# Kernel tuning notes

Measured on AMD Instinct MI355X. Metric: run time of the kernel, lower is better.

Reference implementation:

```python
import jax, jax.numpy as jnp
import numpy as np

# ---- config (matches init_kwargs) ----
VOCAB = 50000
D_MODEL = 256
N_HEADS = 8
N_LAYERS = 2
N_KERNELS = 11
D_FF = 2048  # torch TransformerEncoderLayer default
D_HEAD = D_MODEL // N_HEADS
LN_EPS = 1e-5


def kernel_mus(n):
    mus = [1.0]
    bin_size = 2.0 / (n - 1)
    mus.append(1 - bin_size / 2)
    for i in range(1, n - 1):
        mus.append(mus[i] - bin_size)
    return mus


def kernel_sigmas(n):
    bin_size = 2.0 / (n - 1)
    return [0.0001] + [0.5 * bin_size] * (n - 1)

MU = jnp.asarray(kernel_mus(N_KERNELS), dtype=jnp.float32)      # [K]
SIGMA = jnp.asarray(kernel_sigmas(N_KERNELS), dtype=jnp.float32)  # [K]


def pos_encoding(seq_len, d):
    pos = jnp.arange(seq_len, dtype=jnp.float32)[:, None]
    div = jnp.exp(jnp.arange(0, d, 2, dtype=jnp.float32) * (-np.log(10000.0) / d))
    pe = jnp.zeros((seq_len, d), dtype=jnp.float32)
    pe = pe.at[:, 0::2].set(jnp.sin(pos * div)).at[:, 1::2].set(jnp.cos(pos * div))
    return pe


def layer_norm(x, scale, bias):
    m = jnp.mean(x, axis=-1, keepdims=True)
    v = jnp.mean(jnp.square(x - m), axis=-1, keepdims=True)
    return (x - m) * jax.lax.rsqrt(v + LN_EPS) * scale + bias


def encoder(x, Wqkv, bqkv, Wo, bo, ln1_s, ln1_b, W1, b1, W2, b2, ln2_s, ln2_b):
    # x: [B,S,d]; params stacked over layers on axis 0. Post-LN, ReLU (torch defaults).
    B, S, d = x.shape

    def layer(x, p):
        wqkv, bq, wo, bob, l1s, l1b, w1, b1_, w2, b2_, l2s, l2b = p
        qkv = jnp.einsum('bsd,ed->bse', x, wqkv) + bq          # [B,S,3d]
        q, k, v = jnp.split(qkv, 3, axis=-1)
        def split_heads(t):
            return t.reshape(B, S, N_HEADS, D_HEAD).transpose(0, 2, 1, 3)
        q, k, v = split_heads(q), split_heads(k), split_heads(v)
        scores = jnp.einsum('bhqe,bhke->bhqk', q, k) / np.sqrt(D_HEAD)
        attn = jax.nn.softmax(scores, axis=-1)
        o = jnp.einsum('bhqk,bhke->bhqe', attn, v).transpose(0, 2, 1, 3).reshape(B, S, d)
        o = jnp.einsum('bsd,ed->bse', o, wo) + bob
        x = layer_norm(x + o, l1s, l1b)
        h = jax.nn.relu(jnp.einsum('bsd,fd->bsf', x, w1) + b1_)
        h = jnp.einsum('bsf,df->bsd', h, w2) + b2_
        x = layer_norm(x + h, l2s, l2b)
        return x, None

    x, _ = jax.lax.scan(layer, x, (Wqkv, bqkv, Wo, bo, ln1_s, ln1_b, W1, b1, W2, b2, ln2_s, ln2_b))
    return x


def setup_inputs() -> dict:
    key = jax.random.key(0)
    ks = jax.random.split(key, 16)
    B, Q, D = 256, 32, 256
    inp = {
        'query_ids': jax.random.randint(ks[0], (B, Q), 1, VOCAB),   # >0 so mask is all-ones
        'doc_ids': jax.random.randint(ks[1], (B, D), 1, VOCAB),
        'emb': jax.random.normal(ks[2], (VOCAB, D_MODEL), jnp.float32) * 0.1,
        'a': jnp.full((1, 1, 1), 0.5, jnp.float32),
        'mlp_w': jax.random.normal(ks[3], (1, N_KERNELS), jnp.float32) * 0.1,
        'Wqkv': jax.random.normal(ks[4], (N_LAYERS, 3 * D_MODEL, D_MODEL), jnp.float32) * 0.05,
        'bqkv': jnp.zeros((N_LAYERS, 3 * D_MODEL), jnp.float32),
        'Wo': jax.random.normal(ks[5], (N_LAYERS, D_MODEL, D_MODEL), jnp.float32) * 0.05,
        'bo': jnp.zeros((N_LAYERS, D_MODEL), jnp.float32),
        'ln1_s': jnp.ones((N_LAYERS, D_MODEL), jnp.float32),
        'ln1_b': jnp.zeros((N_LAYERS, D_MODEL), jnp.float32),
        'W1': jax.random.normal(ks[6], (N_LAYERS, D_FF, D_MODEL), jnp.float32) * 0.03,
        'b1': jnp.zeros((N_LAYERS, D_FF), jnp.float32),
        'W2': jax.random.normal(ks[7], (N_LAYERS, D_MODEL, D_FF), jnp.float32) * 0.03,
        'b2': jnp.zeros((N_LAYERS, D_MODEL), jnp.float32),
        'ln2_s': jnp.ones((N_LAYERS, D_MODEL), jnp.float32),
        'ln2_b': jnp.zeros((N_LAYERS, D_MODEL), jnp.float32),
    }
    return inp


def reference(query_ids, doc_ids, emb, a, mlp_w, Wqkv, bqkv, Wo, bo,
              ln1_s, ln1_b, W1, b1, W2, b2, ln2_s, ln2_b):
    enc_p = (Wqkv, bqkv, Wo, bo, ln1_s, ln1_b, W1, b1, W2, b2, ln2_s, ln2_b)
    q_mask = (query_ids > 0).astype(jnp.float32)   # [B,Q]
    d_mask = (doc_ids > 0).astype(jnp.float32)     # [B,D]
    q_emb = emb[query_ids] * q_mask[..., None]     # [B,Q,d]
    d_emb = emb[doc_ids] * d_mask[..., None]       # [B,D,d]
    q_ctx = encoder(2.0 * q_emb + pos_encoding(q_emb.shape[1], D_MODEL)[None], *enc_p)
    d_ctx = encoder(2.0 * d_emb + pos_encoding(d_emb.shape[1], D_MODEL)[None], *enc_p)
    q_mix = (a * q_emb + (1.0 - a) * q_ctx) * q_mask[..., None]
    d_mix = (a * d_emb + (1.0 - a) * d_ctx) * d_mask[..., None]
    sim = jnp.einsum('bqe,bke->bqk', q_mix, d_mix)                    # [B,Q,D]
    K = jnp.exp(-jnp.square(sim[..., None] - MU) / (2.0 * jnp.square(SIGMA)))  # [B,Q,D,K]
    K_masked = K * q_mask[:, :, None, None] * d_mask[:, None, :, None]
    query_kernel = jnp.sum(K_masked, axis=2)                          # [B,Q,K]
    log_qk = jnp.log(jnp.clip(query_kernel, 1e-10, None)) * q_mask[..., None]
    per_kernel = jnp.sum(log_qk, axis=1)                              # [B,K]
    score_log = (per_kernel @ mlp_w.T)[:, 0]
    len_norm = jnp.sum(query_kernel / K_masked.shape[2], axis=1)      # [B,K]
    score_len = (len_norm @ mlp_w.T)[:, 0]
    return score_log + score_len                                      # [B]
```

## Files before the change

### kernel.cpp

```cpp
#include <hip/hip_runtime.h>
#include <math.h>


#define DMODEL 256
typedef float f32x4 __attribute__((ext_vector_type(4)));

__global__ __launch_bounds__(256) void k_pe(float* __restrict__ pe) {
  int s = blockIdx.x, d = threadIdx.x;
  int i2 = d & ~1;
  float freq = expf((float)i2 * (-9.210340371976184f / 256.f));
  float ang = (float)s * freq;
  pe[s * 256 + d] = (d & 1) ? cosf(ang) : sinf(ang);
}

__global__ __launch_bounds__(256) void k_embed(const int* __restrict__ dids,
    const int* __restrict__ qids, const float* __restrict__ emb,
    const float* __restrict__ pe, float* __restrict__ out_x) {
  int tid = threadIdx.x;
  int tok = blockIdx.x * 4 + (tid >> 6);
  int lane = tid & 63;
  int d0 = lane * 4;
  int id, s;
  if (tok < 65536) { id = dids[tok]; s = tok & 255; }
  else             { id = qids[tok - 65536]; s = (tok - 65536) & 31; }
  float m = id > 0 ? 2.f : 0.f;
  float4 e = *(const float4*)(emb + (size_t)id * DMODEL + d0);
  float4 p = *(const float4*)(pe + s * 256 + d0);
  float4 o;
  o.x = m * e.x + p.x; o.y = m * e.y + p.y;
  o.z = m * e.z + p.z; o.w = m * e.w + p.w;
  *(float4*)(out_x + (size_t)tok * DMODEL + d0) = o;
}

template<bool RELU>
__global__ __launch_bounds__(256) void k_gemm(const float* __restrict__ X,
    const float* __restrict__ W, const float* __restrict__ bias,
    float* __restrict__ out, int M, int N, int K) {
  __shared__ float As[2][16][128];
  __shared__ float Bs[2][16][128];
  int n0 = blockIdx.x * 128;
  int m0 = blockIdx.y * 128;
  int tid = threadIdx.x;
  const int wv = tid >> 6, lane = tid & 63;
  const int r8 = lane >> 3, c8 = lane & 7;
  const int R0 = (wv & 1) * 64 + r8 * 4;
  const int C0 = (wv >> 1) * 64 + c8 * 4;
  int lr = tid >> 1;
  int lk = (tid & 1) << 3;
  const float* Xp = X + (size_t)(m0 + lr) * K + lk;
  const float* Wp = W + (size_t)(n0 + lr) * K + lk;

  float acc[8][8];
#pragma unroll
  for (int i = 0; i < 8; ++i)
#pragma unroll
    for (int j = 0; j < 8; ++j) acc[i][j] = 0.f;

  float4 a0, a1, b0, b1;

#define GLOADT(KT) do { \
    a0 = *(const float4*)(Xp + (KT)); a1 = *(const float4*)(Xp + (KT) + 4); \
    b0 = *(const float4*)(Wp + (KT)); b1 = *(const float4*)(Wp + (KT) + 4); } while (0)

#define LWRITE(BUF) do { \
    As[BUF][lk + 0][lr] = a0.x; As[BUF][lk + 1][lr] = a0.y; \
    As[BUF][lk + 2][lr] = a0.z; As[BUF][lk + 3][lr] = a0.w; \
    As[BUF][lk + 4][lr] = a1.x; As[BUF][lk + 5][lr] = a1.y; \
    As[BUF][lk + 6][lr] = a1.z; As[BUF][lk + 7][lr] = a1.w; \
    Bs[BUF][lk + 0][lr] = b0.x; Bs[BUF][lk + 1][lr] = b0.y; \
    Bs[BUF][lk + 2][lr] = b0.z; Bs[BUF][lk + 3][lr] = b0.w; \
    Bs[BUF][lk + 4][lr] = b1.x; Bs[BUF][lk + 5][lr] = b1.y; \
    Bs[BUF][lk + 6][lr] = b1.z; Bs[BUF][lk + 7][lr] = b1.w; } while (0)

#define COMPT(BUF) do { \
    _Pragma("unroll") \
    for (int k = 0; k < 16; ++k) { \
      float av[8], bv[8]; \
      *(float4*)&av[0] = *(const float4*)&As[BUF][k][R0]; \
      *(float4*)&av[4] = *(const float4*)&As[BUF][k][R0 + 32]; \
      *(float4*)&bv[0] = *(const float4*)&Bs[BUF][k][C0]; \
      *(float4*)&bv[4] = *(const float4*)&Bs[BUF][k][C0 + 32]; \
      _Pragma("unroll") \
      for (int i = 0; i < 8; ++i) \
        _Pragma("unroll") \
        for (int j = 0; j < 8; ++j) \
          acc[i][j] += av[i] * bv[j]; \
    } } while (0)

  const int nt = K >> 4;
  GLOADT(0);
  LWRITE(0);
  __syncthreads();
  for (int t = 0; t < nt; t += 2) {
    int k1 = (t + 1) * 16;
    GLOADT(k1);
    COMPT(0);
    LWRITE(1);
    __syncthreads();
    if (t + 2 < nt) {
      int k2 = (t + 2) * 16;
      GLOADT(k2);
      COMPT(1);
      LWRITE(0);
    } else {
      COMPT(1);
    }
    __syncthreads();
  }
#undef GLOADT
#undef LWRITE
#undef COMPT

#pragma unroll
  for (int i = 0; i < 8; ++i) {
    int mr = m0 + (wv & 1) * 64 + ((i < 4) ? (r8 * 4 + i) : (32 + r8 * 4 + i - 4));
#pragma unroll
    for (int jb = 0; jb < 2; ++jb) {
      int nc = n0 + (wv >> 1) * 64 + jb * 32 + c8 * 4;
      float4 bz = *(const float4*)(bias + nc);
      float4 o4;
      o4.x = acc[i][jb * 4 + 0] + bz.x;
      o4.y = acc[i][jb * 4 + 1] + bz.y;
      o4.z = acc[i][jb * 4 + 2] + bz.z;
      o4.w = acc[i][jb * 4 + 3] + bz.w;
      if (RELU) {
        o4.x = fmaxf(o4.x, 0.f); o4.y = fmaxf(o4.y, 0.f);
        o4.z = fmaxf(o4.z, 0.f); o4.w = fmaxf(o4.w, 0.f);
      }
      *(float4*)(out + (size_t)mr * N + nc) = o4;
    }
  }
}

__global__ __launch_bounds__(256) void k_gemm_ln(const float* __restrict__ X,
    const float* __restrict__ W, const float* __restrict__ bias,
    float* __restrict__ xres, const float* __restrict__ lns,
    const float* __restrict__ lnb, int M, int K) {
  __shared__ float As[2][16][64];
  __shared__ float Bs[2][16][256];
  const int tid = threadIdx.x;
  const int m0 = blockIdx.x * 64;
  const int tx = tid & 15, ty = tid >> 4;
  const int rowA = tid & 63;
  const int kqA = (tid >> 6) << 2;
  const float* Xp = X + (size_t)(m0 + rowA) * K + kqA;
  const float* Wp = W + (size_t)tid * K;

  f32x4 acc[4][4];
#pragma unroll
  for (int r = 0; r < 4; ++r)
#pragma unroll
    for (int q = 0; q < 4; ++q) acc[r][q] = 0.f;

  f32x4 a, b0, b1, b2, b3;

#define GL(KT) do { \
    a  = *(const f32x4*)(Xp + (KT)); \
    b0 = *(const f32x4*)(Wp + (KT));      b1 = *(const f32x4*)(Wp + (KT) + 4); \
    b2 = *(const f32x4*)(Wp + (KT) + 8);  b3 = *(const f32x4*)(Wp + (KT) + 12); } while (0)

#define LW(BUF) do { \
    As[BUF][kqA + 0][rowA] = a[0]; As[BUF][kqA + 1][rowA] = a[1]; \
    As[BUF][kqA + 2][rowA] = a[2]; As[BUF][kqA + 3][rowA] = a[3]; \
    Bs[BUF][ 0][tid] = b0[0]; Bs[BUF][ 1][tid] = b0[1]; \
    Bs[BUF][ 2][tid] = b0[2]; Bs[BUF][ 3][tid] = b0[3]; \
    Bs[BUF][ 4][tid] = b1[0]; Bs[BUF][ 5][tid] = b1[1]; \
    Bs[BUF][ 6][tid] = b1[2]; Bs[BUF][ 7][tid] = b1[3]; \
    Bs[BUF][ 8][tid] = b2[0]; Bs[BUF][ 9][tid] = b2[1]; \
    Bs[BUF][10][tid] = b2[2]; Bs[BUF][11][tid] = b2[3]; \
    Bs[BUF][12][tid] = b3[0]; Bs[BUF][13][tid] = b3[1]; \
    Bs[BUF][14][tid] = b3[2]; Bs[BUF][15][tid] = b3[3]; } while (0)

#define CP(BUF) do { \
    _Pragma("unroll") \
    for (int k = 0; k < 16; ++k) { \
      f32x4 av = *(const f32x4*)&As[BUF][k][ty * 4]; \
      f32x4 bv0 = *(const f32x4*)&Bs[BUF][k][tx * 4]; \
      f32x4 bv1 = *(const f32x4*)&Bs[BUF][k][64 + tx * 4]; \
      f32x4 bv2 = *(const f32x4*)&Bs[BUF][k][128 + tx * 4]; \
      f32x4 bv3 = *(const f32x4*)&Bs[BUF][k][192 + tx * 4]; \
      _Pragma("unroll") \
      for (int r = 0; r < 4; ++r) { \
        acc[r][0] += av[r] * bv0; acc[r][1] += av[r] * bv1; \
        acc[r][2] += av[r] * bv2; acc[r][3] += av[r] * bv3; \
      } \
    } } while (0)

  const int nt = K >> 4;
  GL(0);
  LW(0);
  __syncthreads();
  for (int t = 0; t < nt; t += 2) {
    GL((t + 1) * 16);
    CP(0);
    LW(1);
    __syncthreads();
    if (t + 2 < nt) {
      GL((t + 2) * 16);
      CP(1);
      LW(0);
    } else {
      CP(1);
    }
    __syncthreads();
  }
#undef GL
#undef LW
#undef CP

  f32x4 bza[4], sca[4], lba[4];
#pragma unroll
  for (int q = 0; q < 4; ++q) {
    int c = q * 64 + tx * 4;
    bza[q] = *(const f32x4*)(bias + c);
    sca[q] = *(const f32x4*)(lns + c);
    lba[q] = *(const f32x4*)(lnb + c);
  }
#pragma unroll
  for (int r = 0; r < 4; ++r) {
    size_t row = (size_t)m0 + ty * 4 + r;
    f32x4 v[4];
    float ps = 0.f;
#pragma unroll
    for (int q = 0; q < 4; ++q) {
      f32x4 xr = *(const f32x4*)(xres + row * 256 + q * 64 + tx * 4);
      v[q] = acc[r][q] + bza[q] + xr;
      ps += v[q][0] + v[q][1] + v[q][2] + v[q][3];
    }
    ps += __shfl_xor(ps, 1); ps += __shfl_xor(ps, 2);
    ps += __shfl_xor(ps, 4); ps += __shfl_xor(ps, 8);
    float mean = ps * (1.f / 256.f);
    float ss = 0.f;
#pragma unroll
    for (int q = 0; q < 4; ++q) {
      v[q] -= mean;
      ss += v[q][0] * v[q][0] + v[q][1] * v[q][1]
          + v[q][2] * v[q][2] + v[q][3] * v[q][3];
    }
    ss += __shfl_xor(ss, 1); ss += __shfl_xor(ss, 2);
    ss += __shfl_xor(ss, 4); ss += __shfl_xor(ss, 8);
    float rs = rsqrtf(ss * (1.f / 256.f) + 1e-5f);
#pragma unroll
    for (int q = 0; q < 4; ++q) {
      f32x4 y = v[q] * rs * sca[q] + lba[q];
      *(f32x4*)(xres + row * 256 + q * 64 + tx * 4) = y;
    }
  }
}

template<int NR>
__global__ __launch_bounds__(128) void k_attn(const float* __restrict__ qkv,
    float* __restrict__ o, int S, int b0) {
  __shared__ float Ks[256 * 32];
  __shared__ float Vs[256 * 32];
  int bl = blockIdx.x >> 3;
  int h = blockIdx.x & 7;
  int tid = threadIdx.x;
  const float* base = qkv + (size_t)bl * S * 768;
  int hc = h * 32;
  for (int f = tid; f < S * 32; f += 128) {
    int s = f >> 5, e = f & 31;
    Ks[f] = base[(size_t)s * 768 + 256 + hc + e];
    Vs[f] = base[(size_t)s * 768 + 512 + hc + e];
  }
  __syncthreads();
  if (tid >= S) return;
  const float scale = 0.17677669529663687f;
  float q[NR][32], acc[NR][32], m[NR], l[NR];
#pragma unroll
  for (int r = 0; r < NR; ++r) {
    int row = tid + 128 * r;
    const float4* qp = (const float4*)(base + (size_t)row * 768 + hc);
#pragma unroll
    for (int w = 0; w < 8; ++w) {
      float4 t = qp[w];
      q[r][4 * w] = t.x; q[r][4 * w + 1] = t.y; q[r][4 * w + 2] = t.z; q[r][4 * w + 3] = t.w;
    }
    m[r] = -1e30f; l[r] = 0.f;
#pragma unroll
    for (int e = 0; e < 32; ++e) acc[r][e] = 0.f;
  }
  for (int j = 0; j < S; ++j) {
    float kv[32];
    const float4* kp = (const float4*)&Ks[j * 32];
#pragma unroll
    for (int w = 0; w < 8; ++w) {
      float4 t = kp[w];
      kv[4 * w] = t.x; kv[4 * w + 1] = t.y; kv[4 * w + 2] = t.z; kv[4 * w + 3] = t.w;
    }
    float p[NR];
#pragma unroll
    for (int r = 0; r < NR; ++r) {
      float dot = 0.f;
#pragma unroll
      for (int e = 0; e < 32; ++e) dot += q[r][e] * kv[e];
      float s_ = dot * scale;
      float mn = fmaxf(m[r], s_);
      p[r] = __expf(s_ - mn);
      if (mn > m[r]) {
        float al = __expf(m[r] - mn);
        l[r] *= al;
#pragma unroll
        for (int e = 0; e < 32; ++e) acc[r][e] *= al;
        m[r] = mn;
      }
      l[r] += p[r];
    }
    const float4* vp = (const float4*)&Vs[j * 32];
#pragma unroll
    for (int w = 0; w < 8; ++w) {
      float4 t = vp[w];
#pragma unroll
      for (int r = 0; r < NR; ++r) {
        acc[r][4 * w]     += p[r] * t.x;
        acc[r][4 * w + 1] += p[r] * t.y;
        acc[r][4 * w + 2] += p[r] * t.z;
        acc[r][4 * w + 3] += p[r] * t.w;
      }
    }
  }
#pragma unroll
  for (int r = 0; r < NR; ++r) {
    int row = tid + 128 * r;
    float inv = 1.f / l[r];
    float4* op = (float4*)(o + ((size_t)(b0 + bl) * S + row) * DMODEL + hc);
#pragma unroll
    for (int w = 0; w < 8; ++w) {
      float4 t;
      t.x = acc[r][4 * w] * inv;     t.y = acc[r][4 * w + 1] * inv;
      t.z = acc[r][4 * w + 2] * inv; t.w = acc[r][4 * w + 3] * inv;
      op[w] = t;
    }
  }
}

__global__ __launch_bounds__(256) void k_score(
    const int* __restrict__ qids, const int* __restrict__ dids,
    const float* __restrict__ emb, const float* __restrict__ xq,
    const float* __restrict__ xd, const float* __restrict__ a_ptr,
    const float* __restrict__ mlp_w, float* __restrict__ out) {
  __shared__ float qmix[32 * 256];
  __shared__ float qks[32 * 11];
  __shared__ float qmask_s[32];
  int b = blockIdx.x, tid = threadIdx.x;
  float av = a_ptr[0], aw = 1.f - av;
  for (int q = 0; q < 32; ++q) {
    int qid = qids[b * 32 + q];
    float qm = qid > 0 ? 1.f : 0.f;
    float ev = emb[(size_t)qid * 256 + tid];
    float xv = xq[((size_t)b * 32 + q) * 256 + tid];
    qmix[q * 256 + tid] = (av * ev + aw * xv) * qm;
    if (tid == 0) qmask_s[q] = qm;
  }
  for (int i = tid; i < 352; i += 256) qks[i] = 0.f;
  __syncthreads();
  int j = tid;
  int did = dids[b * 256 + j];
  float dmask = did > 0 ? 1.f : 0.f;
  float sim[32];
#pragma unroll
  for (int q = 0; q < 32; ++q) sim[q] = 0.f;
  const float4* de = (const float4*)(emb + (size_t)did * 256);
  const float4* dxp = (const float4*)(xd + ((size_t)b * 256 + j) * 256);
  for (int c = 0; c < 4; ++c) {
    float4 dreg[16];
#pragma unroll
    for (int w = 0; w < 16; ++w) {
      float4 e = de[c * 16 + w], x = dxp[c * 16 + w];
      dreg[w].x = av * e.x + aw * x.x;
      dreg[w].y = av * e.y + aw * x.y;
      dreg[w].z = av * e.z + aw * x.z;
      dreg[w].w = av * e.w + aw * x.w;
    }
#pragma unroll
    for (int q = 0; q < 32; ++q) {
      const float4* qp = (const float4*)&qmix[q * 256 + c * 64];
      float d_ = 0.f;
#pragma unroll
      for (int w = 0; w < 16; ++w) {
        float4 t = qp[w];
        d_ += t.x * dreg[w].x + t.y * dreg[w].y + t.z * dreg[w].z + t.w * dreg[w].w;
      }
      sim[q] += d_;
    }
  }
  const float MU[11] = {1.f, 0.9f, 0.7f, 0.5f, 0.3f, 0.1f, -0.1f, -0.3f, -0.5f, -0.7f, -0.9f};
  const float IC[11] = {5e7f, 50.f, 50.f, 50.f, 50.f, 50.f, 50.f, 50.f, 50.f, 50.f, 50.f};
  for (int q = 0; q < 32; ++q) {
    float s = sim[q];
    float f = dmask * qmask_s[q];
#pragma unroll
    for (int k = 0; k < 11; ++k) {
      float d_ = s - MU[k];
      float v = expf(-d_ * d_ * IC[k]) * f;
#pragma unroll
      for (int o = 32; o > 0; o >>= 1) v += __shfl_xor(v, o);
      if ((tid & 63) == 0) atomicAdd(&qks[q * 11 + k], v);
    }
  }
  __syncthreads();
  if (tid < 32) {
    float qm = qmask_s[tid];
    float p = 0.f;
#pragma unroll
    for (int k = 0; k < 11; ++k) {
      float qv = qks[tid * 11 + k];
      p += mlp_w[k] * (qm * logf(fmaxf(qv, 1e-10f)) + qv * (1.f / 256.f));
    }
#pragma unroll
    for (int o = 16; o > 0; o >>= 1) p += __shfl_xor(p, o);
    if (tid == 0) out[b] = p;
  }
}

extern "C" void kernel_launch(void* const* d_in, const int* in_sizes, int n_in,
                              void* d_out, int out_size, void* d_ws, size_t ws_size,
                              hipStream_t stream) {
  const int* qids = (const int*)d_in[0];
  const int* dids = (const int*)d_in[1];
  const float* emb = (const float*)d_in[2];
  const float* a = (const float*)d_in[3];
  const float* mlp_w = (const float*)d_in[4];
  const float* Wqkv = (const float*)d_in[5];
  const float* bqkv = (const float*)d_in[6];
  const float* Wo = (const float*)d_in[7];
  const float* bo = (const float*)d_in[8];
  const float* l1s = (const float*)d_in[9];
  const float* l1b = (const float*)d_in[10];
  const float* W1 = (const float*)d_in[11];
  const float* b1 = (const float*)d_in[12];
  const float* W2 = (const float*)d_in[13];
  const float* b2 = (const float*)d_in[14];
  const float* l2s = (const float*)d_in[15];
  const float* l2b = (const float*)d_in[16];
  float* out = (float*)d_out;
  float* ws = (float*)d_ws;

  const int TOK = 73728;
  const size_t QRY_QKV = (size_t)8192 * 768;

  size_t wsf = ws_size / 4;
  const size_t fixed = 2 * (size_t)TOK * 256 + 65536;
  const int cbs[] = {256, 128, 64, 32, 16, 8};
  const int fcs[] = {24576, 12288, 9216, 6144, 3072, 2048};
  int CB = 8, FC = 2048;
  for (int i = 0; i < 6; ++i) {
    size_t sc = (size_t)cbs[i] * 196608;
    size_t s2 = (size_t)fcs[i] * 2048;
    size_t scr = sc > s2 ? sc : s2;
    if (scr < QRY_QKV) scr = QRY_QKV;
    if (fixed + scr <= wsf) { CB = cbs[i]; FC = fcs[i]; break; }
  }
  size_t scrN = (size_t)CB * 196608;
  { size_t s2 = (size_t)FC * 2048; if (s2 > scrN) scrN = s2; if (QRY_QKV > scrN) scrN = QRY_QKV; }

  float* x       = ws;
  float* t0      = x + (size_t)TOK * 256;
  float* pe      = t0 + (size_t)TOK * 256;
  float* scratch = pe + 65536;

  k_pe<<<256, 256, 0, stream>>>(pe);
  k_embed<<<TOK / 4, 256, 0, stream>>>(dids, qids, emb, pe, x);

  for (int l = 0; l < 2; ++l) {
    const float* wq = Wqkv + (size_t)l * 768 * 256;
    const float* bq = bqkv + l * 768;
    const float* wo = Wo + (size_t)l * 256 * 256;
    const float* bo_ = bo + l * 256;
    const float* w1 = W1 + (size_t)l * 2048 * 256;
    const float* b1_ = b1 + l * 2048;
    const float* w2 = W2 + (size_t)l * 256 * 2048;
    const float* b2_ = b2 + l * 256;

    for (int c = 0; c < 256; c += CB) {
      int Mc = CB * 256;
      k_gemm<false><<<dim3(6, Mc / 128), 256, 0, stream>>>(
          x + (size_t)c * 65536, wq, bq, scratch, Mc, 768, 256);
      k_attn<2><<<CB * 8, 128, 0, stream>>>(scratch, t0, 256, c);
    }
    k_gemm<false><<<dim3(6, 64), 256, 0, stream>>>(
        x + (size_t)65536 * 256, wq, bq, scratch, 8192, 768, 256);
    k_attn<1><<<256 * 8, 128, 0, stream>>>(scratch, t0 + (size_t)65536 * 256, 32, 0);
    k_gemm_ln<<<TOK / 64, 256, 0, stream>>>(t0, wo, bo_, x,
        l1s + l * 256, l1b + l * 256, TOK, 256);
    for (int f = 0; f < TOK; f += FC) {
      k_gemm<true><<<dim3(16, FC / 128), 256, 0, stream>>>(
          x + (size_t)f * 256, w1, b1_, scratch, FC, 2048, 256);
      k_gemm_ln<<<FC / 64, 256, 0, stream>>>(scratch, w2, b2_, x + (size_t)f * 256,
          l2s + l * 256, l2b + l * 256, FC, 2048);
    }
  }

  k_score<<<256, 256, 0, stream>>>(qids, dids, emb, x + (size_t)65536 * 256,
                                   x, a, mlp_w, out);
}
```

Baseline: 7.185 ms.

## Specialize attention kernels: one row per thread for docs, all heads per block for queries

Replaces the templated attention kernel with two specialized kernels. The document kernel uses 256 threads, one query row each, instead of 128 threads handling two rows, and loads K/V tiles with vectorized f32x4 stores into shared memory. The query kernel handles all 8 heads of a 32-token sequence in one 256-thread block instead of launching one 128-thread block per head with 96 idle threads. Dot products are split across two vector accumulators to shorten dependency chains, at the cost of different register pressure and occupancy.

```diff
diff --git a/kernel.cpp b/kernel.cpp
--- a/kernel.cpp
+++ b/kernel.cpp
@@ -248,90 +248,107 @@
   }
 }
 
-template<int NR>
-__global__ __launch_bounds__(128) void k_attn(const float* __restrict__ qkv,
-    float* __restrict__ o, int S, int b0) {
-  __shared__ float Ks[256 * 32];
-  __shared__ float Vs[256 * 32];
-  int bl = blockIdx.x >> 3;
-  int h = blockIdx.x & 7;
+__global__ __launch_bounds__(256) void k_attn_doc(const float* __restrict__ qkv,
+    float* __restrict__ o, int b0) {
+  __shared__ f32x4 Ks[256 * 8];
+  __shared__ f32x4 Vs[256 * 8];
+  int bl = blockIdx.x >> 3, h = blockIdx.x & 7;
   int tid = threadIdx.x;
-  const float* base = qkv + (size_t)bl * S * 768;
+  const float* base = qkv + (size_t)bl * 256 * 768;
   int hc = h * 32;
-  for (int f = tid; f < S * 32; f += 128) {
-    int s = f >> 5, e = f & 31;
-    Ks[f] = base[(size_t)s * 768 + 256 + hc + e];
-    Vs[f] = base[(size_t)s * 768 + 512 + hc + e];
+  for (int idx = tid; idx < 2048; idx += 256) {
+    int s = idx >> 3, w = idx & 7;
+    Ks[idx] = *(const f32x4*)(base + (size_t)s * 768 + 256 + hc + w * 4);
+    Vs[idx] = *(const f32x4*)(base + (size_t)s * 768 + 512 + hc + w * 4);
   }
   __syncthreads();
-  if (tid >= S) return;
+  f32x4 q[8], acc[8];
+  const float* qp = base + (size_t)tid * 768 + hc;
+#pragma unroll
+  for (int w = 0; w < 8; ++w) { q[w] = *(const f32x4*)(qp + 4 * w); acc[w] = 0.f; }
+  float m = -1e30f, l = 0.f;
   const float scale = 0.17677669529663687f;
-  float q[NR][32], acc[NR][32], m[NR], l[NR];
-#pragma unroll
-  for (int r = 0; r < NR; ++r) {
-    int row = tid + 128 * r;
-    const float4* qp = (const float4*)(base + (size_t)row * 768 + hc);
-#pragma unroll
-    for (int w = 0; w < 8; ++w) {
-      float4 t = qp[w];
-      q[r][4 * w] = t.x; q[r][4 * w + 1] = t.y; q[r][4 * w + 2] = t.z; q[r][4 * w + 3] = t.w;
-    }
-    m[r] = -1e30f; l[r] = 0.f;
-#pragma unroll
-    for (int e = 0; e < 32; ++e) acc[r][e] = 0.f;
-  }
-  for (int j = 0; j < S; ++j) {
-    float kv[32];
-    const float4* kp = (const float4*)&Ks[j * 32];
-#pragma unroll
-    for (int w = 0; w < 8; ++w) {
-      float4 t = kp[w];
-      kv[4 * w] = t.x; kv[4 * w + 1] = t.y; kv[4 * w + 2] = t.z; kv[4 * w + 3] = t.w;
-    }
-    float p[NR];
-#pragma unroll
-    for (int r = 0; r < NR; ++r) {
-      float dot = 0.f;
-#pragma unroll
-      for (int e = 0; e < 32; ++e) dot += q[r][e] * kv[e];
-      float s_ = dot * scale;
-      float mn = fmaxf(m[r], s_);
-      p[r] = __expf(s_ - mn);
-      if (mn > m[r]) {
-        float al = __expf(m[r] - mn);
-        l[r] *= al;
-#pragma unroll
-        for (int e = 0; e < 32; ++e) acc[r][e] *= al;
-        m[r] = mn;
-      }
-      l[r] += p[r];
-    }
-    const float4* vp = (const float4*)&Vs[j * 32];
-#pragma unroll
-    for (int w = 0; w < 8; ++w) {
-      float4 t = vp[w];
-#pragma unroll
-      for (int r = 0; r < NR; ++r) {
-        acc[r][4 * w]     += p[r] * t.x;
-        acc[r][4 * w + 1] += p[r] * t.y;
-        acc[r][4 * w + 2] += p[r] * t.z;
-        acc[r][4 * w + 3] += p[r] * t.w;
-      }
-    }
-  }
-#pragma unroll
-  for (int r = 0; r < NR; ++r) {
-    int row = tid + 128 * r;
-    float inv = 1.f / l[r];
-    float4* op = (float4*)(o + ((size_t)(b0 + bl) * S + row) * DMODEL + hc);
-#pragma unroll
-    for (int w = 0; w < 8; ++w) {
-      float4 t;
-      t.x = acc[r][4 * w] * inv;     t.y = acc[r][4 * w + 1] * inv;
-      t.z = acc[r][4 * w + 2] * inv; t.w = acc[r][4 * w + 3] * inv;
-      op[w] = t;
-    }
-  }
+  for (int j = 0; j < 256; ++j) {
+    const f32x4* kr = &Ks[j * 8];
+    f32x4 da = q[0] * kr[0];
+    f32x4 db = q[1] * kr[1];
+#pragma unroll
+    for (int w = 2; w < 8; w += 2) {
+      da += q[w] * kr[w];
+      db += q[w + 1] * kr[w + 1];
+    }
+    f32x4 d4 = da + db;
+    float s_ = (d4[0] + d4[1] + d4[2] + d4[3]) * scale;
+    float mn = fmaxf(m, s_);
+    float p = __expf(s_ - mn);
+    if (mn > m) {
+      float al = __expf(m - mn);
+      l *= al;
+#pragma unroll
+      for (int w = 0; w < 8; ++w) acc[w] *= al;
+      m = mn;
+    }
+    l += p;
+    const f32x4* vr = &Vs[j * 8];
+#pragma unroll
+    for (int w = 0; w < 8; ++w) acc[w] += p * vr[w];
+  }
+  float inv = 1.f / l;
+  float* op = o + ((size_t)(b0 + bl) * 256 + tid) * DMODEL + hc;
+#pragma unroll
+  for (int w = 0; w < 8; ++w) *(f32x4*)(op + 4 * w) = acc[w] * inv;
+}
+
+__global__ __launch_bounds__(256) void k_attn_qry(const float* __restrict__ qkv,
+    float* __restrict__ o) {
+  __shared__ f32x4 Ks[32 * 64];
+  __shared__ f32x4 Vs[32 * 64];
+  int bl = blockIdx.x;
+  int tid = threadIdx.x;
+  const float* base = qkv + (size_t)bl * 32 * 768;
+  for (int idx = tid; idx < 2048; idx += 256) {
+    int s = idx >> 6, c = idx & 63;
+    Ks[idx] = *(const f32x4*)(base + (size_t)s * 768 + 256 + c * 4);
+    Vs[idx] = *(const f32x4*)(base + (size_t)s * 768 + 512 + c * 4);
+  }
+  __syncthreads();
+  int h = tid >> 5, row = tid & 31;
+  int hc = h * 32;
+  f32x4 q[8], acc[8];
+  const float* qp = base + (size_t)row * 768 + hc;
+#pragma unroll
+  for (int w = 0; w < 8; ++w) { q[w] = *(const f32x4*)(qp + 4 * w); acc[w] = 0.f; }
+  float m = -1e30f, l = 0.f;
+  const float scale = 0.17677669529663687f;
+  for (int j = 0; j < 32; ++j) {
+    const f32x4* kr = &Ks[j * 64 + h * 8];
+    f32x4 da = q[0] * kr[0];
+    f32x4 db = q[1] * kr[1];
+#pragma unroll
+    for (int w = 2; w < 8; w += 2) {
+      da += q[w] * kr[w];
+      db += q[w + 1] * kr[w + 1];
+    }
+    f32x4 d4 = da + db;
+    float s_ = (d4[0] + d4[1] + d4[2] + d4[3]) * scale;
+    float mn = fmaxf(m, s_);
+    float p = __expf(s_ - mn);
+    if (mn > m) {
+      float al = __expf(m - mn);
+      l *= al;
+#pragma unroll
+      for (int w = 0; w < 8; ++w) acc[w] *= al;
+      m = mn;
+    }
+    l += p;
+    const f32x4* vr = &Vs[j * 64 + h * 8];
+#pragma unroll
+    for (int w = 0; w < 8; ++w) acc[w] += p * vr[w];
+  }
+  float inv = 1.f / l;
+  float* op = o + ((size_t)bl * 32 + row) * DMODEL + hc;
+#pragma unroll
+  for (int w = 0; w < 8; ++w) *(f32x4*)(op + 4 * w) = acc[w] * inv;
 }
 
 __global__ __launch_bounds__(256) void k_score(
@@ -451,8 +468,6 @@
     if (scr < QRY_QKV) scr = QRY_QKV;
     if (fixed + scr <= wsf) { CB = cbs[i]; FC = fcs[i]; break; }
   }
-  size_t scrN = (size_t)CB * 196608;
-  { size_t s2 = (size_t)FC * 2048; if (s2 > scrN) scrN = s2; if (QRY_QKV > scrN) scrN = QRY_QKV; }
 
   float* x       = ws;
   float* t0      = x + (size_t)TOK * 256;
@@ -476,11 +491,11 @@
       int Mc = CB * 256;
       k_gemm<false><<<dim3(6, Mc / 128), 256, 0, stream>>>(
           x + (size_t)c * 65536, wq, bq, scratch, Mc, 768, 256);
-      k_attn<2><<<CB * 8, 128, 0, stream>>>(scratch, t0, 256, c);
+      k_attn_doc<<<CB * 8, 256, 0, stream>>>(scratch, t0, c);
     }
     k_gemm<false><<<dim3(6, 64), 256, 0, stream>>>(
         x + (size_t)65536 * 256, wq, bq, scratch, 8192, 768, 256);
-    k_attn<1><<<256 * 8, 128, 0, stream>>>(scratch, t0 + (size_t)65536 * 256, 32, 0);
+    k_attn_qry<<<256, 256, 0, stream>>>(scratch, t0 + (size_t)65536 * 256);
     k_gemm_ln<<<TOK / 64, 256, 0, stream>>>(t0, wo, bo_, x,
         l1s + l * 256, l1b + l * 256, TOK, 256);
     for (int f = 0; f < TOK; f += FC) {
```

New measurement: 6.844 ms. 1.05x faster.
